# Optimization experiments

Hardware: AMD Instinct MI355X
Metric: run time of the kernel (lower is better)

Reference implementation:

```python
import jax, jax.numpy as jnp
import numpy as np

H, DN, DR, DV, L = 16, 128, 64, 128, 512
EPS = 1e-6

def rotate_half(x):
    x1, x2 = jnp.split(x, 2, axis=-1)
    return jnp.concatenate((-x2, x1), axis=-1)

def setup_inputs() -> dict:
    key = jax.random.key(0)
    ks = jax.random.split(key, 8)
    B, S, HID = 2, 2048, 2048
    inv_freq = 1.0 / (10000.0 ** (jnp.arange(0, DR, 2, dtype=jnp.float32) / DR))
    pos = jnp.arange(B * S, dtype=jnp.float32)
    freqs = pos[:, None] * inv_freq[None, :]
    emb = jnp.concatenate((freqs, freqs), axis=-1)
    return {
        "hidden_states": jax.random.normal(ks[0], (B, S, HID), jnp.float32),
        "cos": jnp.cos(emb),
        "sin": jnp.sin(emb),
        "q_proj_w": jax.random.normal(ks[1], (H * (DN + DR), HID), jnp.float32) * 0.02,
        "kv_a_proj_w": jax.random.normal(ks[2], (L + DR, HID), jnp.float32) * 0.02,
        "kv_a_ln_w": jnp.ones((L,), jnp.float32),
        "W_UK_T": jax.random.normal(ks[3], (H, DN, L), jnp.float32) * 0.02,
        "W_UV": jax.random.normal(ks[4], (H, L, DV), jnp.float32) * 0.02,
        "o_proj_w": jax.random.normal(ks[5], (HID, H * DV), jnp.float32) * 0.02,
    }

def reference(hidden_states, cos, sin, q_proj_w, kv_a_proj_w, kv_a_ln_w, W_UK_T, W_UV, o_proj_w):
    B, S, HID = hidden_states.shape
    T = B * S
    x = hidden_states.reshape(T, HID)
    # q projection -> [T, H, DN+DR]
    q = (x @ q_proj_w.T).reshape(T, H, DN + DR)
    q_pass, q_rot = q[..., :DN], q[..., DN:]
    # compressed kv -> latent + rope key (MQA-style, shared across heads)
    ckv = x @ kv_a_proj_w.T  # [T, L+DR]
    k_pass, k_rot = ckv[..., :L], ckv[..., L:]
    kv_c = k_pass * jax.lax.rsqrt(jnp.mean(k_pass * k_pass, axis=-1, keepdims=True) + EPS) * kv_a_ln_w
    # interleaved RoPE (rope_interleave=True): de-interleave then rotate_half form
    q_rot = q_rot.reshape(T, H, DR // 2, 2).swapaxes(-1, -2).reshape(T, H, DR)
    k_rot = k_rot.reshape(T, DR // 2, 2).swapaxes(-1, -2).reshape(T, DR)
    q_rot = q_rot * cos[:, None, :] + rotate_half(q_rot) * sin[:, None, :]
    k_rot = k_rot * cos + rotate_half(k_rot) * sin
    # absorb W_UK into queries: [T,H,L]
    q_lat = jnp.einsum('thd,hdl->thl', q_pass, W_UK_T)
    q_lat = q_lat.reshape(B, S, H, L)
    q_rot = q_rot.reshape(B, S, H, DR)
    kv_c_b = kv_c.reshape(B, S, L)
    k_rot_b = k_rot.reshape(B, S, DR)
    scale = 1.0 / np.sqrt(DN + DR)
    scores = (jnp.einsum('bshl,btl->bhst', q_lat, kv_c_b)
              + jnp.einsum('bshd,btd->bhst', q_rot, k_rot_b)) * scale
    causal = jnp.tril(jnp.ones((S, S), dtype=bool))
    scores = jnp.where(causal[None, None], scores, jnp.float32(-1e30))
    attn = jax.nn.softmax(scores, axis=-1)
    out_lat = jnp.einsum('bhst,btl->bshl', attn, kv_c_b)   # [B,S,H,L]
    out = jnp.einsum('bshl,hlv->bshv', out_lat, W_UV)       # [B,S,H,DV]
    out = out.reshape(B, S, H * DV) @ o_proj_w.T
    return out
```

## Files before the change

### kernel.cpp

```cpp
#include <hip/hip_runtime.h>
#include <stdint.h>

#define T_TOK 4096
#define HIDD  2048
#define NH    16
#define DNN   128
#define DRR   64
#define DVV   128
#define LAT   512
#define DQK   576
#define SEQ   2048
#define NB    2
#define KSTR  592
#define KCH   2368
#define QCKV  3712

typedef __attribute__((__ext_vector_type__(8))) short short8;
typedef __attribute__((__ext_vector_type__(4))) float f32x4;

__device__ __forceinline__ float bf2f(ushort u) {
  union { uint32_t i; float f; } v; v.i = ((uint32_t)u) << 16; return v.f;
}
__device__ __forceinline__ ushort f2bf(float f) {
  union { float f; uint32_t i; } v; v.f = f;
  uint32_t r = v.i + 0x7FFF + ((v.i >> 16) & 1);
  return (ushort)(r >> 16);
}

__device__ __forceinline__ void gld_lds16(const void* g, void* l) {
  __builtin_amdgcn_global_load_lds((const __attribute__((address_space(1))) void*)g,
                                   (__attribute__((address_space(3))) void*)l, 16, 0, 0);
}

__global__ void cast4(const float* __restrict__ in, ushort* __restrict__ out, int n4) {
  int i = blockIdx.x * blockDim.x + threadIdx.x;
  if (i >= n4) return;
  float4 v = ((const float4*)in)[i];
  ushort4 o; o.x = f2bf(v.x); o.y = f2bf(v.y); o.z = f2bf(v.z); o.w = f2bf(v.w);
  ((ushort4*)out)[i] = o;
}

__global__ void cast_pad_kv(const float* __restrict__ in, ushort* __restrict__ out) {
  int i = blockIdx.x * 256 + threadIdx.x;
  int row = (i * 4) >> 11;
  ushort4 o;
  if (row < 576) {
    float4 v = ((const float4*)in)[i];
    o.x = f2bf(v.x); o.y = f2bf(v.y); o.z = f2bf(v.z); o.w = f2bf(v.w);
  } else { o.x = 0; o.y = 0; o.z = 0; o.w = 0; }
  ((ushort4*)out)[i] = o;
}

__global__ void cast_wuk(const float* __restrict__ in, ushort* __restrict__ out) {
  int o = blockIdx.x * 256 + threadIdx.x;
  int d = o & 127, l = (o >> 7) & 511, h = o >> 16;
  out[o] = f2bf(in[((size_t)(h * 128 + d)) * 512 + l]);
}
__global__ void cast_wuv(const float* __restrict__ in, ushort* __restrict__ out) {
  int o = blockIdx.x * 256 + threadIdx.x;
  int l = o & 511, v = (o >> 9) & 127, h = o >> 16;
  out[o] = f2bf(in[((size_t)(h * 512 + l)) * 128 + v]);
}

template<int OUT_BF16>
__global__ __launch_bounds__(256) void gemm_bt(
    const ushort* __restrict__ A, const ushort* __restrict__ B, void* __restrict__ Cv,
    int K, int lda, int ldb, int ldc,
    long long aB, long long bB, long long cB)
{
  __shared__ ushort As[2][128 * 32];
  __shared__ ushort Bs[2][128 * 32];
  const int tid = threadIdx.x;
  const int lane = tid & 63, wid = tid >> 6;
  const int m0 = blockIdx.y * 128, n0 = blockIdx.x * 128;
  A += (size_t)blockIdx.z * aB;
  B += (size_t)blockIdx.z * bB;
  const int wm = (wid >> 1) * 64, wn = (wid & 1) * 64;
  const int fr = lane & 15;
  const int kk = (lane >> 4) * 8;

  auto stage = [&](int k0, int buf) {
#pragma unroll
    for (int i = 0; i < 2; ++i) {
      int c = i * 256 + tid;
      gld_lds16(A + (size_t)(m0 + (c >> 2)) * lda + k0 + (c & 3) * 8, (void*)(&As[buf][0] + c * 8));
    }
#pragma unroll
    for (int i = 0; i < 2; ++i) {
      int c = i * 256 + tid;
      gld_lds16(B + (size_t)(n0 + (c >> 2)) * ldb + k0 + (c & 3) * 8, (void*)(&Bs[buf][0] + c * 8));
    }
  };

  f32x4 acc[4][4] = {};
  const int nt = K >> 5;
  stage(0, 0);
  for (int t = 0; t < nt; ++t) {
    const int cur = t & 1;
    if (t + 1 < nt) {
      stage((t + 1) << 5, cur ^ 1);
      asm volatile("s_waitcnt vmcnt(4)" ::: "memory");
    } else {
      asm volatile("s_waitcnt vmcnt(0)" ::: "memory");
    }
    __builtin_amdgcn_sched_barrier(0);
    __builtin_amdgcn_s_barrier();
    __builtin_amdgcn_sched_barrier(0);

    short8 af[4], bf[4];
#pragma unroll
    for (int x = 0; x < 4; ++x) af[x] = *(const short8*)(&As[cur][0] + (wm + x * 16 + fr) * 32 + kk);
#pragma unroll
    for (int x = 0; x < 4; ++x) bf[x] = *(const short8*)(&Bs[cur][0] + (wn + x * 16 + fr) * 32 + kk);
#pragma unroll
    for (int mi = 0; mi < 4; ++mi)
#pragma unroll
      for (int ni = 0; ni < 4; ++ni)
        acc[mi][ni] = __builtin_amdgcn_mfma_f32_16x16x32_bf16(af[mi], bf[ni], acc[mi][ni], 0, 0, 0);

    __builtin_amdgcn_sched_barrier(0);
    __builtin_amdgcn_s_barrier();
    __builtin_amdgcn_sched_barrier(0);
  }

  const int rb = (lane >> 4) * 4;
#pragma unroll
  for (int mi = 0; mi < 4; ++mi)
#pragma unroll
    for (int ni = 0; ni < 4; ++ni)
#pragma unroll
      for (int r = 0; r < 4; ++r) {
        size_t row = (size_t)(m0 + wm + mi * 16 + rb + r);
        size_t col = (size_t)(n0 + wn + ni * 16 + fr);
        size_t idx = row * (size_t)ldc + col + (size_t)blockIdx.z * cB;
        if (OUT_BF16) ((ushort*)Cv)[idx] = f2bf(acc[mi][ni][r]);
        else          ((float*)Cv)[idx]  = acc[mi][ni][r];
      }
}

__global__ __launch_bounds__(256) void rms_rope_k(
    const ushort* __restrict__ qckv, const float* __restrict__ lnw,
    const float* __restrict__ cosb, const float* __restrict__ sinb,
    ushort* __restrict__ k_eff)
{
  const int t = blockIdx.x, tid = threadIdx.x;
  __shared__ float red[4];
  const size_t base = (size_t)t * QCKV + 3072;
  float v0 = bf2f(qckv[base + tid]);
  float v1 = bf2f(qckv[base + 256 + tid]);
  float ss = v0 * v0 + v1 * v1;
#pragma unroll
  for (int m = 1; m < 64; m <<= 1) ss += __shfl_xor(ss, m);
  if ((tid & 63) == 0) red[tid >> 6] = ss;
  __syncthreads();
  float rn = rsqrtf((red[0] + red[1] + red[2] + red[3]) * (1.0f / 512.0f) + 1e-6f);
  k_eff[(size_t)t * KSTR + tid]       = f2bf(v0 * rn * lnw[tid]);
  k_eff[(size_t)t * KSTR + 256 + tid] = f2bf(v1 * rn * lnw[256 + tid]);
  if (tid < 64) {
    int j = tid;
    int src  = (j < 32) ? 2 * j : 2 * (j - 32) + 1;
    int psrc = (j < 32) ? src + 1 : src - 1;
    float xv = bf2f(qckv[base + 512 + src]);
    float pv = bf2f(qckv[base + 512 + psrc]);
    float c = cosb[t * 64 + j], s = sinb[t * 64 + j];
    k_eff[(size_t)t * KSTR + 512 + j] = f2bf((j < 32) ? xv * c - pv * s : xv * c + pv * s);
  }
}

__global__ __launch_bounds__(256) void transpose_kv(
    const ushort* __restrict__ keff, ushort* __restrict__ kvT)
{
  __shared__ ushort Tl[64][72];
  const int s0 = blockIdx.x * 64, v0 = blockIdx.y * 64, b = blockIdx.z;
  const int tid = threadIdx.x;
#pragma unroll
  for (int i = 0; i < 2; ++i) {
    int c = i * 256 + tid;
    int r = c >> 3, c8 = (c & 7) * 8;
    *(short8*)&Tl[r][c8] = *(const short8*)&keff[((size_t)b * SEQ + s0 + r) * KSTR + v0 + c8];
  }
  __syncthreads();
#pragma unroll
  for (int i = 0; i < 2; ++i) {
    int c = i * 256 + tid;
    int v = c >> 3, s8 = (c & 7) * 8;
    short8 o;
#pragma unroll
    for (int e = 0; e < 8; ++e) o[e] = Tl[s8 + e][v];
    *(short8*)&kvT[((size_t)b * 512 + v0 + v) * SEQ + s0 + s8] = o;
  }
}

__global__ void rope_q(const ushort* __restrict__ qb, const float* __restrict__ cosb,
                       const float* __restrict__ sinb, ushort* __restrict__ q_eff)
{
  const int t = blockIdx.x;
  const int h = blockIdx.y * 4 + threadIdx.y;
  const int j = threadIdx.x;
  size_t base = (size_t)t * QCKV + h * 192 + 128;
  int src  = (j < 32) ? 2 * j : 2 * (j - 32) + 1;
  int psrc = (j < 32) ? src + 1 : src - 1;
  float xv = bf2f(qb[base + src]), pv = bf2f(qb[base + psrc]);
  float c = cosb[t * 64 + j], s = sinb[t * 64 + j];
  q_eff[((size_t)h * T_TOK + t) * DQK + 512 + j] = f2bf((j < 32) ? xv * c - pv * s : xv * c + pv * s);
}

__global__ __launch_bounds__(512, 2) void attn3(
    const ushort* __restrict__ q_eff, const ushort* __restrict__ keff,
    const ushort* __restrict__ kvT, ushort* __restrict__ out_lat)
{
  const int pair = blockIdx.x;
  const int h = blockIdx.y, b = blockIdx.z;
  const int tid = threadIdx.x, lane = tid & 63, w = tid >> 6;
  __shared__ ushort Ks[2][32 * KSTR];
  __shared__ ushort Vt[2][512 * 32];
  __shared__ ushort Pl[8][16 * 40];

  const int fr = lane & 15, g = lane >> 4;

  auto stageK = [&](int kt, int buf) {
    const ushort* ksrc = keff + ((size_t)b * SEQ + (size_t)kt * 32) * KSTR;
    ushort* kd = &Ks[buf][0];
#pragma unroll
    for (int i = 0; i < 5; ++i) {
      int c0 = w * 320 + i * 64;
      if (c0 < KCH) {
        int c = c0 + lane;
        gld_lds16(ksrc + (size_t)c * 8, (void*)(kd + (size_t)c * 8));
      }
    }
  };
  auto stageV = [&](int kt, int buf) {
    const ushort* vsrc = kvT + (size_t)b * 512 * SEQ + (size_t)kt * 32;
    ushort* vd = &Vt[buf][0];
#pragma unroll
    for (int i = 0; i < 4; ++i) {
      int c = w * 256 + i * 64 + lane;
      gld_lds16(vsrc + (size_t)(c >> 2) * SEQ + (c & 3) * 8, (void*)(vd + (size_t)c * 8));
    }
  };

  for (int half = 0; half < 2; ++half) {
    const int qb = half ? pair : (15 - pair);
    const int q0 = qb * 128 + w * 16;

    const ushort* qrow = q_eff + ((size_t)h * T_TOK + (size_t)b * SEQ + q0 + fr) * DQK + g * 8;
    short8 qf[18];
#pragma unroll
    for (int ks = 0; ks < 18; ++ks) qf[ks] = *(const short8*)(qrow + ks * 32);

    f32x4 acc[32] = {};
    float m_s[4] = {-1e30f, -1e30f, -1e30f, -1e30f};
    float l_s[4] = {0.f, 0.f, 0.f, 0.f};

    const int nt = 4 * qb + 4;

    stageK(0, 0);
    stageV(0, 0);

    for (int kt = 0; kt < nt; ++kt) {
      const int cur = kt & 1;
      if (kt + 1 < nt) {
        stageK(kt + 1, cur ^ 1);
        stageV(kt + 1, cur ^ 1);
        if (w == 7) asm volatile("s_waitcnt vmcnt(6)" ::: "memory");
        else        asm volatile("s_waitcnt vmcnt(9)" ::: "memory");
      } else {
        asm volatile("s_waitcnt vmcnt(0)" ::: "memory");
      }
      __builtin_amdgcn_sched_barrier(0);
      __builtin_amdgcn_s_barrier();
      __builtin_amdgcn_sched_barrier(0);

      if (kt * 32 <= q0 + 15) {
        const ushort* Kc = &Ks[cur][0];
        const ushort* Vc = &Vt[cur][0];
        f32x4 s0 = {}, s1 = {};
#pragma unroll
        for (int ks = 0; ks < 18; ++ks) {
          short8 b0 = *(const short8*)(Kc + (0 * 16 + fr) * KSTR + ks * 32 + g * 8);
          short8 b1 = *(const short8*)(Kc + (1 * 16 + fr) * KSTR + ks * 32 + g * 8);
          s0 = __builtin_amdgcn_mfma_f32_16x16x32_bf16(qf[ks], b0, s0, 0, 0, 0);
          s1 = __builtin_amdgcn_mfma_f32_16x16x32_bf16(qf[ks], b1, s1, 0, 0, 0);
        }
        const float SC = 0.07216878364870322f;
        const bool diag = (kt * 32 + 31 > q0);
        float sv0[4], sv1[4];
#pragma unroll
        for (int r = 0; r < 4; ++r) {
          int qg = q0 + 4 * g + r;
          float a0 = s0[r] * SC, a1 = s1[r] * SC;
          if (diag) {
            if (kt * 32 + fr > qg)      a0 = -1e30f;
            if (kt * 32 + 16 + fr > qg) a1 = -1e30f;
          }
          sv0[r] = a0; sv1[r] = a1;
        }
        float mx[4];
#pragma unroll
        for (int r = 0; r < 4; ++r) {
          float m2 = fmaxf(sv0[r], sv1[r]);
          m2 = fmaxf(m2, __shfl_xor(m2, 1));
          m2 = fmaxf(m2, __shfl_xor(m2, 2));
          m2 = fmaxf(m2, __shfl_xor(m2, 4));
          m2 = fmaxf(m2, __shfl_xor(m2, 8));
          mx[r] = m2;
        }
        float need = mx[0] - m_s[0];
#pragma unroll
        for (int r = 1; r < 4; ++r) need = fmaxf(need, mx[r] - m_s[r]);
        if (__any(need > 8.0f)) {
          float rsc[4];
#pragma unroll
          for (int r = 0; r < 4; ++r) {
            float mn = fmaxf(m_s[r], mx[r]);
            rsc[r] = __expf(m_s[r] - mn);
            m_s[r] = mn;
            l_s[r] *= rsc[r];
          }
#pragma unroll
          for (int n2 = 0; n2 < 32; ++n2)
#pragma unroll
            for (int r = 0; r < 4; ++r) acc[n2][r] *= rsc[r];
        }
        float p0[4], p1[4];
#pragma unroll
        for (int r = 0; r < 4; ++r) {
          p0[r] = __expf(sv0[r] - m_s[r]);
          p1[r] = __expf(sv1[r] - m_s[r]);
          float ps = p0[r] + p1[r];
          ps += __shfl_xor(ps, 1);
          ps += __shfl_xor(ps, 2);
          ps += __shfl_xor(ps, 4);
          ps += __shfl_xor(ps, 8);
          l_s[r] += ps;
          Pl[w][(4 * g + r) * 40 + fr]      = f2bf(p0[r]);
          Pl[w][(4 * g + r) * 40 + 16 + fr] = f2bf(p1[r]);
        }
        short8 pa = *(const short8*)(Pl[w] + fr * 40 + g * 8);
#pragma unroll
        for (int n2 = 0; n2 < 32; ++n2) {
          short8 bv = *(const short8*)(Vc + (n2 * 16 + fr) * 32 + g * 8);
          acc[n2] = __builtin_amdgcn_mfma_f32_16x16x32_bf16(pa, bv, acc[n2], 0, 0, 0);
        }
      }
      __builtin_amdgcn_sched_barrier(0);
      __builtin_amdgcn_s_barrier();
      __builtin_amdgcn_sched_barrier(0);
    }

    const size_t obase = ((size_t)h * T_TOK + (size_t)b * SEQ + q0) * LAT;
    float inv[4];
#pragma unroll
    for (int r = 0; r < 4; ++r) inv[r] = 1.0f / l_s[r];
#pragma unroll
    for (int n2 = 0; n2 < 32; ++n2)
#pragma unroll
      for (int r = 0; r < 4; ++r)
        out_lat[obase + (size_t)(4 * g + r) * LAT + n2 * 16 + fr] = f2bf(acc[n2][r] * inv[r]);
  }
}

extern "C" void kernel_launch(void* const* d_in, const int* in_sizes, int n_in,
                              void* d_out, int out_size, void* d_ws, size_t ws_size,
                              hipStream_t stream) {
  const float* hs   = (const float*)d_in[0];
  const float* cosb = (const float*)d_in[1];
  const float* sinb = (const float*)d_in[2];
  const float* qw   = (const float*)d_in[3];
  const float* kvw  = (const float*)d_in[4];
  const float* lnw  = (const float*)d_in[5];
  const float* wuk  = (const float*)d_in[6];
  const float* wuv  = (const float*)d_in[7];
  const float* wo   = (const float*)d_in[8];
  float* out = (float*)d_out;
  char* ws = (char*)d_ws;

  const size_t o_xb   = 0;
  const size_t o_qb   = 16777216;
  const size_t o_wq   = 47185920;
  const size_t o_wkv  = 59768832;
  const size_t o_ol   = 0;
  const size_t o_wukt = 67108864;
  const size_t o_wuvt = 69206016;
  const size_t o_wo   = 71303168;
  const size_t o_keff = 79691776;
  const size_t o_qeff = 84541440;
  const size_t o_oh   = 160038912;
  const size_t o_kvt  = 176816128;

  ushort* xb    = (ushort*)(ws + o_xb);
  ushort* qbuf  = (ushort*)(ws + o_qb);
  ushort* wq_b  = (ushort*)(ws + o_wq);
  ushort* wkv_b = (ushort*)(ws + o_wkv);
  ushort* olat  = (ushort*)(ws + o_ol);
  ushort* wukt  = (ushort*)(ws + o_wukt);
  ushort* wuvt  = (ushort*)(ws + o_wuvt);
  ushort* wo_b  = (ushort*)(ws + o_wo);
  ushort* keff  = (ushort*)(ws + o_keff);
  ushort* qeff  = (ushort*)(ws + o_qeff);
  ushort* ohead = (ushort*)(ws + o_oh);
  ushort* kvt   = (ushort*)(ws + o_kvt);

  cast4<<<8192, 256, 0, stream>>>(hs, xb, 8388608 / 4);
  cast4<<<6144, 256, 0, stream>>>(qw, wq_b, 6291456 / 4);
  cast_pad_kv<<<1280, 256, 0, stream>>>(kvw, wkv_b);
  cast4<<<4096, 256, 0, stream>>>(wo, wo_b, 4194304 / 4);
  cast_wuk<<<4096, 256, 0, stream>>>(wuk, wukt);
  cast_wuv<<<4096, 256, 0, stream>>>(wuv, wuvt);

  gemm_bt<1><<<dim3(29, 32, 1), 256, 0, stream>>>(xb, wq_b, qbuf, 2048, 2048, 2048, QCKV, 0, 0, 0);
  rms_rope_k<<<4096, 256, 0, stream>>>(qbuf, lnw, cosb, sinb, keff);
  transpose_kv<<<dim3(32, 8, 2), 256, 0, stream>>>(keff, kvt);
  rope_q<<<dim3(4096, 4, 1), dim3(64, 4, 1), 0, stream>>>(qbuf, cosb, sinb, qeff);
  gemm_bt<1><<<dim3(4, 32, 16), 256, 0, stream>>>(qbuf, wukt, qeff, 128, QCKV, 128, 576,
                                                  192LL, 65536LL, 2359296LL);
  attn3<<<dim3(8, 16, 2), 512, 0, stream>>>(qeff, keff, kvt, olat);
  gemm_bt<1><<<dim3(1, 32, 16), 256, 0, stream>>>(olat, wuvt, ohead, 512, 512, 512, 2048,
                                                  2097152LL, 65536LL, 128LL);
  gemm_bt<0><<<dim3(16, 32, 1), 256, 0, stream>>>(ohead, wo_b, out, 2048, 2048, 2048, 2048, 0, 0, 0);
}
```

Baseline: 662.3 us.

## Stage V through registers with XOR-swizzled LDS layout and pad K stride

The V tile is no longer loaded straight into LDS with global_load_lds. It is loaded into registers, then written to LDS with an XOR swizzle on the 8-element column chunks so the MFMA B-operand reads avoid bank conflicts. The K row stride grows from 592 to 600 elements, with zero-filled padding, to change its bank mapping. The V register writes are interleaved after the QK/softmax phase to overlap with compute. This adds VGPR pressure and manual waitcnt bookkeeping that must stay correct.

```diff
diff --git a/kernel.cpp b/kernel.cpp
--- a/kernel.cpp
+++ b/kernel.cpp
@@ -11,8 +11,8 @@
 #define DQK   576
 #define SEQ   2048
 #define NB    2
-#define KSTR  592
-#define KCH   2368
+#define KSTR  600
+#define KCH   2400
 #define QCKV  3712
 
 typedef __attribute__((__ext_vector_type__(8))) short short8;
@@ -164,6 +164,8 @@
     float pv = bf2f(qckv[base + 512 + psrc]);
     float c = cosb[t * 64 + j], s = sinb[t * 64 + j];
     k_eff[(size_t)t * KSTR + 512 + j] = f2bf((j < 32) ? xv * c - pv * s : xv * c + pv * s);
+  } else if (tid < 88) {
+    k_eff[(size_t)t * KSTR + 512 + tid] = 0;
   }
 }
 
@@ -217,6 +219,9 @@
   __shared__ ushort Pl[8][16 * 40];
 
   const int fr = lane & 15, g = lane >> 4;
+  const int e_r = (fr >> 1) & 3;
+
+  short8 vreg[4];
 
   auto stageK = [&](int kt, int buf) {
     const ushort* ksrc = keff + ((size_t)b * SEQ + (size_t)kt * 32) * KSTR;
@@ -226,17 +231,25 @@
       int c0 = w * 320 + i * 64;
       if (c0 < KCH) {
         int c = c0 + lane;
-        gld_lds16(ksrc + (size_t)c * 8, (void*)(kd + (size_t)c * 8));
+        if (c < KCH) gld_lds16(ksrc + (size_t)c * 8, (void*)(kd + (size_t)c * 8));
       }
     }
   };
-  auto stageV = [&](int kt, int buf) {
+  auto issueV = [&](int kt) {
     const ushort* vsrc = kvT + (size_t)b * 512 * SEQ + (size_t)kt * 32;
-    ushort* vd = &Vt[buf][0];
 #pragma unroll
     for (int i = 0; i < 4; ++i) {
       int c = w * 256 + i * 64 + lane;
-      gld_lds16(vsrc + (size_t)(c >> 2) * SEQ + (c & 3) * 8, (void*)(vd + (size_t)c * 8));
+      vreg[i] = *(const short8*)(vsrc + (size_t)(c >> 2) * SEQ + (c & 3) * 8);
+    }
+  };
+  auto writeV = [&](int buf) {
+    ushort* vd = &Vt[buf][0];
+#pragma unroll
+    for (int i = 0; i < 4; ++i) {
+      int c = w * 256 + i * 64 + lane;
+      int v = c >> 2, sc = c & 3;
+      *(short8*)(vd + (size_t)v * 32 + ((sc ^ ((v >> 1) & 3)) << 3)) = vreg[i];
     }
   };
 
@@ -255,15 +268,24 @@
 
     const int nt = 4 * qb + 4;
 
+    issueV(0);
+    __builtin_amdgcn_sched_barrier(0);
     stageK(0, 0);
-    stageV(0, 0);
+    __builtin_amdgcn_sched_barrier(0);
+    if (w == 7) asm volatile("s_waitcnt vmcnt(3)" ::: "memory");
+    else        asm volatile("s_waitcnt vmcnt(5)" ::: "memory");
+    __builtin_amdgcn_sched_barrier(0);
+    writeV(0);
+    asm volatile("s_waitcnt lgkmcnt(0)" ::: "memory");
 
     for (int kt = 0; kt < nt; ++kt) {
       const int cur = kt & 1;
       if (kt + 1 < nt) {
+        issueV(kt + 1);
+        __builtin_amdgcn_sched_barrier(0);
         stageK(kt + 1, cur ^ 1);
-        stageV(kt + 1, cur ^ 1);
-        if (w == 7) asm volatile("s_waitcnt vmcnt(6)" ::: "memory");
+        __builtin_amdgcn_sched_barrier(0);
+        if (w == 7) asm volatile("s_waitcnt vmcnt(7)" ::: "memory");
         else        asm volatile("s_waitcnt vmcnt(9)" ::: "memory");
       } else {
         asm volatile("s_waitcnt vmcnt(0)" ::: "memory");
@@ -272,9 +294,9 @@
       __builtin_amdgcn_s_barrier();
       __builtin_amdgcn_sched_barrier(0);
 
-      if (kt * 32 <= q0 + 15) {
+      const bool active = (kt * 32 <= q0 + 15);
+      if (active) {
         const ushort* Kc = &Ks[cur][0];
-        const ushort* Vc = &Vt[cur][0];
         f32x4 s0 = {}, s1 = {};
 #pragma unroll
         for (int ks = 0; ks < 18; ++ks) {
@@ -337,13 +359,23 @@
           Pl[w][(4 * g + r) * 40 + fr]      = f2bf(p0[r]);
           Pl[w][(4 * g + r) * 40 + 16 + fr] = f2bf(p1[r]);
         }
+      }
+      if (kt + 1 < nt) {
+        if (w == 7) asm volatile("s_waitcnt vmcnt(3)" ::: "memory");
+        else        asm volatile("s_waitcnt vmcnt(5)" ::: "memory");
+        __builtin_amdgcn_sched_barrier(0);
+        writeV(cur ^ 1);
+      }
+      if (active) {
+        const ushort* Vc = &Vt[cur][0];
         short8 pa = *(const short8*)(Pl[w] + fr * 40 + g * 8);
 #pragma unroll
         for (int n2 = 0; n2 < 32; ++n2) {
-          short8 bv = *(const short8*)(Vc + (n2 * 16 + fr) * 32 + g * 8);
+          short8 bv = *(const short8*)(Vc + (n2 * 16 + fr) * 32 + ((g ^ e_r) << 3));
           acc[n2] = __builtin_amdgcn_mfma_f32_16x16x32_bf16(pa, bv, acc[n2], 0, 0, 0);
         }
       }
+      asm volatile("s_waitcnt lgkmcnt(0)" ::: "memory");
       __builtin_amdgcn_sched_barrier(0);
       __builtin_amdgcn_s_barrier();
       __builtin_amdgcn_sched_barrier(0);
@@ -385,9 +417,9 @@
   const size_t o_wuvt = 69206016;
   const size_t o_wo   = 71303168;
   const size_t o_keff = 79691776;
-  const size_t o_qeff = 84541440;
-  const size_t o_oh   = 160038912;
-  const size_t o_kvt  = 176816128;
+  const size_t o_qeff = 84606976;
+  const size_t o_oh   = 160104448;
+  const size_t o_kvt  = 176881664;
 
   ushort* xb    = (ushort*)(ws + o_xb);
   ushort* qbuf  = (ushort*)(ws + o_qb);
```

Result: slower. 741.1 us (+11.9%).
